# Performance work log

Hardware: AMD Instinct MI355X
Metric: run time of the kernel (lower is better)

The kernel has to match this reference:

```python
import jax, jax.numpy as jnp
import numpy as np

B, P, N, H, W = 8, 4096, 1024, 1024, 1024


def setup_inputs() -> dict:
    key = jax.random.key(0)
    k1, k2, k3, k4 = jax.random.split(key, 4)
    return {
        "pred_points": jax.random.uniform(k1, (B, P, 2), dtype=jnp.float32),
        "dicts_coords": jax.random.uniform(k2, (B, N, 2), dtype=jnp.float32),
        "dicts_keys": jax.random.randint(k3, (B, N), 0, 1024, dtype=jnp.int64) if jax.config.jax_enable_x64 else jax.random.randint(k3, (B, N), 0, 1024).astype(jnp.int32),
        "masks": jax.random.randint(k4, (B, H, W), 0, 1025).astype(jnp.int32),
    }


def _match_single(U, V, keys, lm):
    # U: [P,2] normalized points, V: [N,2] gt coords, keys: [N] ids, lm: [H,W] label map
    h, w = lm.shape
    x = jnp.clip(jnp.round(U[:, 0] * h).astype(jnp.int32), 0, h - 1)
    y = jnp.clip(jnp.round(U[:, 1] * w).astype(jnp.int32), 0, w - 1)
    labels = lm[x, y]                                   # [P] label at each point
    # inside[j, p] == (mask for gt j covers point p); mask j is label channel keys[j]+1
    inside = labels[None, :] == (keys + 1)[:, None]     # [N,P] bool
    # full euclidean distance matrix gt->points
    D = jnp.sqrt(jnp.sum((V[:, None, :] - U[None, :, :]) ** 2, axis=-1))  # [N,P]
    inside_any = inside.any(axis=0)                     # points inside ANY mask
    avail0 = inside_any
    bg0 = ~inside_any                                   # background points
    idx = jnp.arange(U.shape[0])
    BIG = jnp.asarray(1e30, D.dtype)

    def step(carry, xs):
        avail, bg = carry
        ins_j, d_j = xs
        cand = ins_j & avail
        cnt = cand.sum()
        d_in = jnp.where(cand, d_j, BIG)
        u_in = jnp.argmin(d_in)                         # first-index tiebreak, like list order
        d_bg = jnp.where(bg, d_j, BIG)
        u_bg = jnp.argmin(d_bg)
        has_bg = bg.any()
        use_in = cnt > 0
        u = jnp.where(use_in, u_in, jnp.where(has_bg, u_bg, -1))
        cost = jnp.where(use_in, d_in[u_in], jnp.where(has_bg, d_bg[u_bg], jnp.asarray(0.0, D.dtype)))
        # inside-match consumes u from available; multi-point case dumps others into bg
        avail = jnp.where(use_in, avail & (idx != u_in), avail)
        others = cand & (idx != u_in)
        bg = jnp.where(use_in,
                       jnp.where(cnt > 1, bg | others, bg),
                       jnp.where(has_bg, bg & (idx != u_bg), bg))
        return (avail, bg), (u, cost)

    _, (src, costs) = jax.lax.scan(step, (avail0, bg0), (inside, D))
    tgt = jnp.where(src >= 0, jnp.arange(V.shape[0]), -1)
    return src, tgt, costs.sum()


def reference(pred_points, dicts_coords, dicts_keys, masks):
    # Returns padded matches per batch: src[b,j] = matched point index for gt j (-1 if skipped),
    # tgt[b,j] = j when matched else -1, total_cost[b] = sum of matched distances.
    src, tgt, total_cost = jax.vmap(_match_single)(pred_points, dicts_coords, dicts_keys, masks)
    return src, tgt, total_cost
```

## Files before the change

### kernel.cpp

```cpp
#include <hip/hip_runtime.h>
#include <stdint.h>

#define PPTS 4096
#define NGT  1024
#define HH   1024
#define WW   1024
#define EVPOOL_CAP 3072
#define BGCAP 160
#define RB 12

#define PART_BYTES (8 * 8 * 1025 * 2)
#define LAB_OFF    PART_BYTES
#define SPILL_OFF  (LAB_OFF + 8 * PPTS * 2)
#define SPILL_CAP  2048
#define WS_NEED    (SPILL_OFF + 8 * SPILL_CAP * 2)

typedef unsigned long long u64;

__device__ __forceinline__ float pdist(float vx, float vy, float ux, float uy) {
    float dx = __fsub_rn(vx, ux);
    float dy = __fsub_rn(vy, uy);
    return __fsqrt_rn(__fadd_rn(__fmul_rn(dx, dx), __fmul_rn(dy, dy)));
}

__global__ __launch_bounds__(512) void label_kernel(
    const float* __restrict__ pred, const int* __restrict__ masks,
    unsigned short* __restrict__ part, unsigned short* __restrict__ labs)
{
    __shared__ int lh[1025];
    const int blk = blockIdx.x, b = blk >> 3, sb = blk & 7;
    const int t = threadIdx.x;
    lh[t] = 0; lh[t + 512] = 0;
    if (t == 0) lh[1024] = 0;
    __syncthreads();
    const int p = (sb << 9) + t;
    float2 u = ((const float2*)(pred + (size_t)b * PPTS * 2))[p];
    int xi = (int)rintf(__fmul_rn(u.x, 1024.0f));
    int yi = (int)rintf(__fmul_rn(u.y, 1024.0f));
    xi = min(max(xi, 0), HH - 1);
    yi = min(max(yi, 0), WW - 1);
    int lab = (masks + (size_t)b * HH * WW)[xi * WW + yi];
    labs[(size_t)b * PPTS + p] = (unsigned short)lab;
    atomicAdd(&lh[lab], 1);
    __syncthreads();
    unsigned short* Pp = part + (size_t)b * 8200 + sb * 1025;
    Pp[t] = (unsigned short)lh[t];
    Pp[t + 512] = (unsigned short)lh[t + 512];
    if (t == 0) Pp[1024] = (unsigned short)lh[1024];
}

__global__ __launch_bounds__(1024) void matcher_kernel(
    const float* __restrict__ pred,
    const float* __restrict__ coords,
    const int*   __restrict__ keys,
    const int*   __restrict__ masks,
    float* __restrict__ out,
    const unsigned short* __restrict__ part, const unsigned short* __restrict__ labs,
    unsigned short* __restrict__ spill, int useWs, int B)
{
    __shared__ __align__(16) char regU[32768];
    __shared__ __align__(8)  char regE[8192];
    __shared__ __align__(8)  char regB[8200];
    __shared__ __align__(8)  char regP[2 * EVPOOL_CAP];
    __shared__ __align__(4)  char regS[384];
    __shared__ __align__(8)  char regT[2048];
    __shared__ u64            wScr64[16];
    __shared__ u64            sTot;
    __shared__ unsigned short evAx[1024];
    __shared__ unsigned short occList[NGT];
    __shared__ short          matchU[NGT];
    __shared__ unsigned       bgbits[PPTS / 32];
    __shared__ int            scal[4];

    float2*         bucketC  = (float2*)regU;
    unsigned short* ldsEnt   = (unsigned short*)regE;
    int*            bEnd     = (int*)regB;
    int*            occA     = ((int*)regB) + 1025;
    u64*            specWin  = (u64*)regB;
    int*            firstOcc = (int*)regP;
    unsigned short* evPool   = (unsigned short*)regP;
    unsigned*       present  = (unsigned*)regS;
    unsigned short* bgListSh = (unsigned short*)regS;
    unsigned short* bSt      = (unsigned short*)regT;
    float2*         vSteps   = (float2*)regT;
    int*   wScrI = (int*)wScr64;
    float* wScrF = (float*)wScr64;

    const int b = blockIdx.x;
    const int t = threadIdx.x;
    const int lane = t & 63, wv = t >> 6;
    const float* Ub = pred   + (size_t)b * PPTS * 2;
    const float2* Ub2 = (const float2*)Ub;
    const float* Vb = coords + (size_t)b * NGT * 2;
    const float2* Vb2 = (const float2*)Vb;
    const int*   Kb = keys   + (size_t)b * NGT;
    unsigned short* evSpillB = spill + (size_t)b * SPILL_CAP;
    const int spillCap = useWs ? SPILL_CAP : 0;

    if (t < PPTS / 32) bgbits[t] = 0;
    if (t == 0) scal[0] = 0;
    const int k1 = Kb[t] + 1;
    const float2 vMe = Vb2[t];
    int lab[4]; float2 up[4];
    #pragma unroll
    for (int i = 0; i < 4; i++) up[i] = Ub2[t + (i << 10)];
    occA[t] = 0; firstOcc[t] = 0x7FFFFFFF;
    if (t == 0) { occA[1024] = 0; firstOcc[1024] = 0x7FFFFFFF; }
    if (t < 33) present[t] = 0;
    if (useWs) {
        const unsigned short* Pb = part + (size_t)b * 8200;
        int s = 0;
        #pragma unroll
        for (int sb = 0; sb < 8; sb++) s += Pb[sb * 1025 + t];
        bEnd[t] = s;
        if (t == 0) {
            int s2 = 0;
            #pragma unroll
            for (int sb = 0; sb < 8; sb++) s2 += Pb[sb * 1025 + 1024];
            bEnd[1024] = s2;
        }
        const unsigned short* Lb = labs + (size_t)b * PPTS;
        #pragma unroll
        for (int i = 0; i < 4; i++) lab[i] = Lb[t + (i << 10)];
    } else {
        bEnd[t] = 0;
        if (t == 0) bEnd[1024] = 0;
    }
    __syncthreads();
    atomicOr(&present[k1 >> 5], 1u << (k1 & 31));
    atomicAdd(&occA[k1], 1);
    atomicMin(&firstOcc[k1], t);
    if (!useWs) {
        const int* Mb = masks + (size_t)b * HH * WW;
        #pragma unroll
        for (int i = 0; i < 4; i++) {
            float2 u = up[i];
            int xi = (int)rintf(__fmul_rn(u.x, 1024.0f));
            int yi = (int)rintf(__fmul_rn(u.y, 1024.0f));
            xi = min(max(xi, 0), HH - 1);
            yi = min(max(yi, 0), WW - 1);
            lab[i] = Mb[xi * WW + yi];
            atomicAdd(&bEnd[lab[i]], 1);
        }
    }
    __syncthreads();

    {
        int c0 = bEnd[t], o0 = occA[t];
        bool pr0 = (present[t >> 5] >> (t & 31)) & 1u;
        int bCnt = bEnd[k1];
        int fo   = firstOcc[k1];
        int evc  = (fo == t && bCnt > 0) ? (bCnt - 1) : 0;
        u64 myv = (pr0 ? ((u64)(unsigned)c0 << 32) : ((u64)(unsigned)c0 << 48))
                  | ((u64)(unsigned)evc << 16) | (u64)(unsigned)o0;
        u64 add1 = 0; bool pr1 = false;
        if (t == 1023) {
            int c1 = bEnd[1024], o1 = occA[1024];
            pr1 = present[32] & 1u;
            add1 = (pr1 ? ((u64)(unsigned)c1 << 32) : ((u64)(unsigned)c1 << 48))
                   | (u64)(unsigned)o1;
        }
        u64 tot = myv + add1;
        u64 inc = tot;
        #pragma unroll
        for (int off = 1; off < 64; off <<= 1) {
            u64 n = __shfl_up(inc, off, 64);
            if (lane >= off) inc += n;
        }
        if (lane == 63) wScr64[wv] = inc;
        __syncthreads();
        if (t < 16) {
            u64 v = wScr64[t], inc2 = v;
            #pragma unroll
            for (int off = 1; off < 16; off <<= 1) {
                u64 n = __shfl_up(inc2, off, 64);
                if (t >= off) inc2 += n;
            }
            wScr64[t] = inc2 - v;
            if (t == 15) sTot = inc2;
        }
        __syncthreads();
        u64 excl = wScr64[wv] + inc - tot;
        int nBg0v = (int)(sTot >> 48);
        int bgS = (int)(excl >> 48);
        int prS = (int)((excl >> 32) & 0xFFFF);
        int evS = (int)((excl >> 16) & 0xFFFF);
        int ocS = (int)(excl & 0xFFFF);
        int start0 = pr0 ? (nBg0v + prS) : bgS;
        bEnd[t] = start0;
        occA[t] = ocS;
        evAx[t] = (unsigned short)evS;
        if (t >= 1) bSt[t - 1] = (unsigned short)start0;
        if (t == 1023) {
            u64 ex1 = excl + myv;
            int bgS1 = (int)(ex1 >> 48);
            int prS1 = (int)((ex1 >> 32) & 0xFFFF);
            int start1 = pr1 ? (nBg0v + prS1) : bgS1;
            bEnd[1024] = start1; occA[1024] = (int)(ex1 & 0xFFFF);
            bSt[1023] = (unsigned short)start1;
        }
    }
    __syncthreads();
    const int nBg0  = (int)(sTot >> 48);
    const int totEv = (int)((sTot >> 16) & 0xFFFF);
    const int EVcap = min(EVPOOL_CAP, PPTS - nBg0);

    #pragma unroll
    for (int i = 0; i < 4; i++) {
        int p = t + (i << 10);
        int slot = atomicAdd(&bEnd[lab[i]], 1);
        ldsEnt[slot] = (unsigned short)p;
        bucketC[slot] = up[i];
    }
    {
        int slot = atomicAdd(&occA[k1], 1);
        occList[slot] = (unsigned short)t;
    }
    __syncthreads();

    float costPartial = 0.0f;
    {
        const int l = t + 1;
        const int os = occA[t], oe = occA[l];
        for (int i = os + 1; i < oe; i++) {
            unsigned short v = occList[i];
            int k = i - 1;
            while (k >= os && occList[k] > v) { occList[k + 1] = occList[k]; k--; }
            occList[k + 1] = v;
        }
        const int bs = bSt[t], be = bEnd[l];
        const int bn = be - bs;
        if (oe > os && bn > 0 && bn <= RB) {
            float rcx[RB], rcy[RB]; int rp[RB];
            #pragma unroll
            for (int k = 0; k < RB; k++)
                if (k < bn) { float2 c = bucketC[bs + k]; rcx[k] = c.x; rcy[k] = c.y;
                              rp[k] = ldsEnt[bs + k]; }
            unsigned cons = 0;
            for (int o = os; o < oe; o++) {
                int j = occList[o];
                float2 v = ((const float2*)Vb)[j];
                u64 best = ~0ull;
                #pragma unroll
                for (int k = 0; k < RB; k++) {
                    if (k < bn && !((cons >> k) & 1u)) {
                        float d = pdist(v.x, v.y, rcx[k], rcy[k]);
                        u64 pk = ((u64)__float_as_uint(d) << 24)
                                 | ((u64)(unsigned)rp[k] << 12) | (u64)(unsigned)k;
                        if (pk < best) best = pk;
                    }
                }
                if (best != ~0ull) {
                    int eW = (int)(best & 0xFFFull);
                    matchU[j] = (short)((best >> 12) & 0xFFFull);
                    costPartial = __fadd_rn(costPartial,
                                            __uint_as_float((unsigned)(best >> 24)));
                    cons |= 1u << eW;
                    if (o == os) {
                        int base = evAx[j];
                        #pragma unroll
                        for (int k = 0; k < RB; k++) {
                            if (k < bn && k != eW) {
                                int idx = base + k - (k > eW ? 1 : 0);
                                if (idx < EVcap) evPool[idx] = (unsigned short)(bs + k);
                                else if (idx - EVcap < spillCap)
                                    evSpillB[idx - EVcap] = (unsigned short)rp[k];
                            }
                        }
                    }
                } else matchU[j] = -2;
            }
        } else if (oe > os) {
            u64 cons = 0;
            for (int o = os; o < oe; o++) {
                int j = occList[o];
                float2 v = ((const float2*)Vb)[j];
                u64 best = ~0ull;
                int avail = 0;
                for (int e = bs; e < be; e++) {
                    int eIdx = e - bs;
                    int p = ldsEnt[e];
                    bool consd;
                    if (eIdx < 64) consd = (cons >> eIdx) & 1ull;
                    else {
                        consd = false;
                        for (int o2 = os; o2 < o; o2++)
                            if ((int)matchU[occList[o2]] == p) { consd = true; break; }
                    }
                    if (consd) continue;
                    avail++;
                    float2 u = bucketC[e];
                    float d = pdist(v.x, v.y, u.x, u.y);
                    u64 pk = ((u64)__float_as_uint(d) << 24) | ((u64)(unsigned)p << 12)
                             | (u64)(unsigned)eIdx;
                    if (pk < best) best = pk;
                }
                if (avail > 0) {
                    int eW = (int)(best & 0xFFFull);
                    matchU[j] = (short)((best >> 12) & 0xFFFull);
                    costPartial = __fadd_rn(costPartial,
                                            __uint_as_float((unsigned)(best >> 24)));
                    if (eW < 64) cons |= 1ull << eW;
                    if (o == os) {
                        int base = evAx[j], w3 = 0;
                        for (int e = bs; e < be; e++) {
                            if (e - bs == eW) continue;
                            int idx = base + w3;
                            if (idx < EVcap) evPool[idx] = (unsigned short)e;
                            else if (idx - EVcap < spillCap)
                                evSpillB[idx - EVcap] = ldsEnt[e];
                            w3++;
                        }
                    }
                } else matchU[j] = -2;
            }
        }
    }
    __syncthreads();

    {
        bool need = (matchU[t] == (short)-2);
        u64 m = __ballot(need);
        if (lane == 0) wScrI[wv] = __popcll(m);
    }
    __syncthreads();
    if (t < 64) {
        int orig = (t < 16) ? wScrI[t] : 0;
        int v = orig;
        #pragma unroll
        for (int off = 1; off <= 8; off <<= 1) {
            int n = __shfl_up(v, off, 64);
            if (t >= off) v += n;
        }
        if (t < 16) wScrI[t] = v - orig;
        if (t == 15) scal[0] = v;
    }
    __syncthreads();
    {
        bool need = (matchU[t] == (short)-2);
        u64 m = __ballot(need);
        if (need) {
            int rank = __popcll(m & ((1ull << lane) - 1ull));
            int idx = wScrI[wv] + rank;
            if (idx < BGCAP) { bgListSh[idx] = (unsigned short)t; vSteps[idx] = vMe; }
        }
    }
    __syncthreads();

    const int bgCnt = min(scal[0], BGCAP);
    {
        const int nStage = min(totEv, EVcap);
        float2 sc[4]; unsigned short sp[4];
        #pragma unroll
        for (int k = 0; k < 4; k++) {
            int i = t + (k << 10);
            if (i < nStage) { int slot = evPool[i]; sp[k] = ldsEnt[slot]; sc[k] = bucketC[slot]; }
        }
        __syncthreads();
        #pragma unroll
        for (int k = 0; k < 4; k++) {
            int i = t + (k << 10);
            if (i < nStage) { ldsEnt[nBg0 + i] = sp[k]; bucketC[nBg0 + i] = sc[k]; }
        }
    }
    __syncthreads();

    for (int s0 = wv; s0 < bgCnt; s0 += 80) {
        u64 best[5]; float vxq[5], vyq[5]; int limq[5];
        int maxLim = 0;
        #pragma unroll
        for (int q = 0; q < 5; q++) {
            int s = s0 + 16 * q;
            best[q] = ~0ull; limq[q] = 0; vxq[q] = 0.0f; vyq[q] = 0.0f;
            if (s < bgCnt) {
                int js = bgListSh[s];
                float2 v = vSteps[s];
                vxq[q] = v.x; vyq[q] = v.y;
                limq[q] = nBg0 + min((int)evAx[js], EVcap);
                maxLim = max(maxLim, limq[q]);
            }
        }
        for (int i = lane; i < maxLim; i += 64) {
            float2 c = bucketC[i];
            unsigned p = ldsEnt[i];
            #pragma unroll
            for (int q = 0; q < 5; q++) {
                if (i < limq[q]) {
                    float d = pdist(vxq[q], vyq[q], c.x, c.y);
                    u64 pk = ((u64)__float_as_uint(d) << 32) | p;
                    if (pk < best[q]) best[q] = pk;
                }
            }
        }
        #pragma unroll
        for (int q = 0; q < 5; q++) {
            int s = s0 + 16 * q;
            if (s < bgCnt) {
                int js = bgListSh[s];
                int ne = evAx[js];
                u64 bq = best[q];
                for (int ei = EVcap + lane; ei < ne; ei += 64) {
                    if (ei - EVcap >= spillCap) break;
                    unsigned p = evSpillB[ei - EVcap];
                    float2 c = Ub2[p];
                    float d = pdist(vxq[q], vyq[q], c.x, c.y);
                    u64 pk = ((u64)__float_as_uint(d) << 32) | p;
                    if (pk < bq) bq = pk;
                }
                #pragma unroll
                for (int off = 32; off >= 1; off >>= 1) {
                    u64 o = __shfl_xor(bq, off, 64);
                    if (o < bq) bq = o;
                }
                if (lane == 0) specWin[s] = bq;
            }
        }
    }
    __syncthreads();

    {
        int done = 0;
        for (;;) {
            if (t == 0) scal[3] = bgCnt;
            __syncthreads();
            if (t >= done && t < bgCnt) {
                u64 w = specWin[t];
                if (w != ~0ull) {
                    unsigned p = (unsigned)(w & 0xFFFFFFFFull);
                    bool inval = (bgbits[p >> 5] >> (p & 31)) & 1u;
                    if (!inval) {
                        for (int s2 = done; s2 < t; s2++) {
                            u64 w2 = specWin[s2];
                            if (w2 != ~0ull &&
                                (unsigned)(w2 & 0xFFFFFFFFull) == p) { inval = true; break; }
                        }
                    }
                    if (inval) atomicMin(&scal[3], t);
                }
            }
            __syncthreads();
            const int fs = scal[3];
            if (fs >= bgCnt) break;
            if (t >= done && t < fs) {
                u64 w = specWin[t];
                if (w != ~0ull) {
                    unsigned p = (unsigned)(w & 0xFFFFFFFFull);
                    atomicOr(&bgbits[p >> 5], 1u << (p & 31));
                }
            }
            __syncthreads();
            {
                const int js = bgListSh[fs];
                const float2 v = vSteps[fs];
                const int ne = evAx[js];
                const int lim = nBg0 + min(ne, EVcap);
                u64 best = ~0ull;
                for (int i = t; i < lim; i += 1024) {
                    unsigned p = ldsEnt[i];
                    if (!((bgbits[p >> 5] >> (p & 31)) & 1u)) {
                        float2 c = bucketC[i];
                        float d = pdist(v.x, v.y, c.x, c.y);
                        u64 pk = ((u64)__float_as_uint(d) << 32) | p;
                        if (pk < best) best = pk;
                    }
                }
                for (int ei = EVcap + t; ei < ne; ei += 1024) {
                    if (ei - EVcap >= spillCap) break;
                    unsigned p = evSpillB[ei - EVcap];
                    if (!((bgbits[p >> 5] >> (p & 31)) & 1u)) {
                        float2 c = Ub2[p];
                        float d = pdist(v.x, v.y, c.x, c.y);
                        u64 pk = ((u64)__float_as_uint(d) << 32) | p;
                        if (pk < best) best = pk;
                    }
                }
                #pragma unroll
                for (int off = 32; off >= 1; off >>= 1) {
                    u64 o = __shfl_xor(best, off, 64);
                    if (o < best) best = o;
                }
                if (lane == 0) wScr64[wv] = best;
                __syncthreads();
                if (t == 0) {
                    u64 bb = wScr64[0];
                    for (int i = 1; i < 16; i++) if (wScr64[i] < bb) bb = wScr64[i];
                    specWin[fs] = bb;
                    if (bb != ~0ull) {
                        unsigned p = (unsigned)(bb & 0xFFFFFFFFull);
                        bgbits[p >> 5] |= 1u << (p & 31);
                    }
                }
            }
            done = fs + 1;
        }
    }
    if (t < bgCnt) {
        const int js = bgListSh[t];
        u64 w0 = specWin[t];
        if (w0 == ~0ull) matchU[js] = -1;
        else {
            matchU[js] = (short)(w0 & 0xFFFFFFFFull);
            costPartial = __fadd_rn(costPartial, __uint_as_float((unsigned)(w0 >> 32)));
        }
    }
    __syncthreads();

    {
        float cp = costPartial;
        #pragma unroll
        for (int off = 32; off >= 1; off >>= 1) cp += __shfl_xor(cp, off, 64);
        if (lane == 0) wScrF[wv] = cp;
    }
    __syncthreads();
    if (t == 0) {
        float tot = 0.0f;
        for (int i = 0; i < 16; ++i) tot = __fadd_rn(tot, wScrF[i]);
        out[(size_t)2 * B * NGT + b] = tot;
    }
    {
        int u = matchU[t];
        out[(size_t)b * NGT + t] = (float)u;
        out[(size_t)B * NGT + (size_t)b * NGT + t] = (u >= 0) ? (float)t : -1.0f;
    }
}

extern "C" void kernel_launch(void* const* d_in, const int* in_sizes, int n_in,
                              void* d_out, int out_size, void* d_ws, size_t ws_size,
                              hipStream_t stream) {
    const float* pred   = (const float*)d_in[0];
    const float* coords = (const float*)d_in[1];
    const int*   keys   = (const int*)d_in[2];
    const int*   masks  = (const int*)d_in[3];
    float* out = (float*)d_out;
    int B = in_sizes[2] / NGT;
    int useWs = (B == 8 && ws_size >= (size_t)WS_NEED) ? 1 : 0;
    unsigned short* partP  = (unsigned short*)d_ws;
    unsigned short* labsP  = (unsigned short*)((char*)d_ws + LAB_OFF);
    unsigned short* spillP = (unsigned short*)((char*)d_ws + SPILL_OFF);
    if (useWs) {
        label_kernel<<<B * 8, 512, 0, stream>>>(pred, masks, partP, labsP);
    }
    matcher_kernel<<<B, 1024, 0, stream>>>(pred, coords, keys, masks, out,
                                           partP, labsP, spillP, useWs, B);
}
```

Measured before the change: 130.2 us.

## Compare squared distances in argmin searches and cache gt coords in LDS

All nearest-point searches now rank candidates by squared distance and apply sqrt only to the winning cost, which removes a correctly rounded sqrt from every inner-loop candidate. GT coordinates are staged into shared memory so the per-bucket matching loops read from LDS instead of global memory. The background speculative loop now gives each wave five consecutive steps instead of steps strided by 16. Ranking by squared distance can resolve ties differently from the reference when two distinct squared values round to the same sqrt result, which could change which index wins.

```diff
diff --git a/kernel.cpp b/kernel.cpp
--- a/kernel.cpp
+++ b/kernel.cpp
@@ -17,10 +17,10 @@
 
 typedef unsigned long long u64;
 
-__device__ __forceinline__ float pdist(float vx, float vy, float ux, float uy) {
+__device__ __forceinline__ float pdist2(float vx, float vy, float ux, float uy) {
     float dx = __fsub_rn(vx, ux);
     float dy = __fsub_rn(vy, uy);
-    return __fsqrt_rn(__fadd_rn(__fmul_rn(dx, dx), __fmul_rn(dy, dy)));
+    return __fadd_rn(__fmul_rn(dx, dx), __fmul_rn(dy, dy));
 }
 
 __global__ __launch_bounds__(512) void label_kernel(
@@ -71,6 +71,7 @@
     __shared__ short          matchU[NGT];
     __shared__ unsigned       bgbits[PPTS / 32];
     __shared__ int            scal[4];
+    __shared__ float2         vLds[NGT];
 
     float2*         bucketC  = (float2*)regU;
     unsigned short* ldsEnt   = (unsigned short*)regE;
@@ -101,6 +102,7 @@
     if (t == 0) scal[0] = 0;
     const int k1 = Kb[t] + 1;
     const float2 vMe = Vb2[t];
+    vLds[t] = vMe;
     int lab[4]; float2 up[4];
     #pragma unroll
     for (int i = 0; i < 4; i++) up[i] = Ub2[t + (i << 10)];
@@ -239,13 +241,13 @@
             unsigned cons = 0;
             for (int o = os; o < oe; o++) {
                 int j = occList[o];
-                float2 v = ((const float2*)Vb)[j];
+                float2 v = vLds[j];
                 u64 best = ~0ull;
                 #pragma unroll
                 for (int k = 0; k < RB; k++) {
                     if (k < bn && !((cons >> k) & 1u)) {
-                        float d = pdist(v.x, v.y, rcx[k], rcy[k]);
-                        u64 pk = ((u64)__float_as_uint(d) << 24)
+                        float d2 = pdist2(v.x, v.y, rcx[k], rcy[k]);
+                        u64 pk = ((u64)__float_as_uint(d2) << 24)
                                  | ((u64)(unsigned)rp[k] << 12) | (u64)(unsigned)k;
                         if (pk < best) best = pk;
                     }
@@ -254,7 +256,7 @@
                     int eW = (int)(best & 0xFFFull);
                     matchU[j] = (short)((best >> 12) & 0xFFFull);
                     costPartial = __fadd_rn(costPartial,
-                                            __uint_as_float((unsigned)(best >> 24)));
+                        __fsqrt_rn(__uint_as_float((unsigned)(best >> 24))));
                     cons |= 1u << eW;
                     if (o == os) {
                         int base = evAx[j];
@@ -274,7 +276,7 @@
             u64 cons = 0;
             for (int o = os; o < oe; o++) {
                 int j = occList[o];
-                float2 v = ((const float2*)Vb)[j];
+                float2 v = vLds[j];
                 u64 best = ~0ull;
                 int avail = 0;
                 for (int e = bs; e < be; e++) {
@@ -290,8 +292,8 @@
                     if (consd) continue;
                     avail++;
                     float2 u = bucketC[e];
-                    float d = pdist(v.x, v.y, u.x, u.y);
-                    u64 pk = ((u64)__float_as_uint(d) << 24) | ((u64)(unsigned)p << 12)
+                    float d2 = pdist2(v.x, v.y, u.x, u.y);
+                    u64 pk = ((u64)__float_as_uint(d2) << 24) | ((u64)(unsigned)p << 12)
                              | (u64)(unsigned)eIdx;
                     if (pk < best) best = pk;
                 }
@@ -299,7 +301,7 @@
                     int eW = (int)(best & 0xFFFull);
                     matchU[j] = (short)((best >> 12) & 0xFFFull);
                     costPartial = __fadd_rn(costPartial,
-                                            __uint_as_float((unsigned)(best >> 24)));
+                        __fsqrt_rn(__uint_as_float((unsigned)(best >> 24))));
                     if (eW < 64) cons |= 1ull << eW;
                     if (o == os) {
                         int base = evAx[j], w3 = 0;
@@ -365,12 +367,12 @@
     }
     __syncthreads();
 
-    for (int s0 = wv; s0 < bgCnt; s0 += 80) {
+    for (int base5 = wv * 5; base5 < bgCnt; base5 += 80) {
         u64 best[5]; float vxq[5], vyq[5]; int limq[5];
         int maxLim = 0;
         #pragma unroll
         for (int q = 0; q < 5; q++) {
-            int s = s0 + 16 * q;
+            int s = base5 + q;
             best[q] = ~0ull; limq[q] = 0; vxq[q] = 0.0f; vyq[q] = 0.0f;
             if (s < bgCnt) {
                 int js = bgListSh[s];
@@ -386,15 +388,15 @@
             #pragma unroll
             for (int q = 0; q < 5; q++) {
                 if (i < limq[q]) {
-                    float d = pdist(vxq[q], vyq[q], c.x, c.y);
-                    u64 pk = ((u64)__float_as_uint(d) << 32) | p;
+                    float d2 = pdist2(vxq[q], vyq[q], c.x, c.y);
+                    u64 pk = ((u64)__float_as_uint(d2) << 32) | p;
                     if (pk < best[q]) best[q] = pk;
                 }
             }
         }
         #pragma unroll
         for (int q = 0; q < 5; q++) {
-            int s = s0 + 16 * q;
+            int s = base5 + q;
             if (s < bgCnt) {
                 int js = bgListSh[s];
                 int ne = evAx[js];
@@ -403,8 +405,8 @@
                     if (ei - EVcap >= spillCap) break;
                     unsigned p = evSpillB[ei - EVcap];
                     float2 c = Ub2[p];
-                    float d = pdist(vxq[q], vyq[q], c.x, c.y);
-                    u64 pk = ((u64)__float_as_uint(d) << 32) | p;
+                    float d2 = pdist2(vxq[q], vyq[q], c.x, c.y);
+                    u64 pk = ((u64)__float_as_uint(d2) << 32) | p;
                     if (pk < bq) bq = pk;
                 }
                 #pragma unroll
@@ -459,8 +461,8 @@
                     unsigned p = ldsEnt[i];
                     if (!((bgbits[p >> 5] >> (p & 31)) & 1u)) {
                         float2 c = bucketC[i];
-                        float d = pdist(v.x, v.y, c.x, c.y);
-                        u64 pk = ((u64)__float_as_uint(d) << 32) | p;
+                        float d2 = pdist2(v.x, v.y, c.x, c.y);
+                        u64 pk = ((u64)__float_as_uint(d2) << 32) | p;
                         if (pk < best) best = pk;
                     }
                 }
@@ -469,8 +471,8 @@
                     unsigned p = evSpillB[ei - EVcap];
                     if (!((bgbits[p >> 5] >> (p & 31)) & 1u)) {
                         float2 c = Ub2[p];
-                        float d = pdist(v.x, v.y, c.x, c.y);
-                        u64 pk = ((u64)__float_as_uint(d) << 32) | p;
+                        float d2 = pdist2(v.x, v.y, c.x, c.y);
+                        u64 pk = ((u64)__float_as_uint(d2) << 32) | p;
                         if (pk < best) best = pk;
                     }
                 }
@@ -500,7 +502,8 @@
         if (w0 == ~0ull) matchU[js] = -1;
         else {
             matchU[js] = (short)(w0 & 0xFFFFFFFFull);
-            costPartial = __fadd_rn(costPartial, __uint_as_float((unsigned)(w0 >> 32)));
+            costPartial = __fadd_rn(costPartial,
+                __fsqrt_rn(__uint_as_float((unsigned)(w0 >> 32))));
         }
     }
     __syncthreads();
```

Measured after the change: 119.5 us. 1.09x faster.
